# Performance work log

Measured on AMD Instinct MI355X. Metric: run time of the kernel, lower is better.

The kernel has to match this reference:

```python
import jax, jax.numpy as jnp
import numpy as np

NEG_SLOPE = 0.2  # PyG GATv2Conv default negative_slope


def gatv2_conv(x, src, dst, Wl, Wr, att, bias, concat):
    # x: [N, Fin]; src/dst: [E]; Wl/Wr: [Fin, H*C]; att: [H, C]
    N = x.shape[0]
    H, C = att.shape
    xl = (x @ Wl).reshape(N, H, C)
    xr = (x @ Wr).reshape(N, H, C)
    m = jax.nn.leaky_relu(xl[src] + xr[dst], NEG_SLOPE)          # [E,H,C]
    logits = jnp.einsum('ehc,hc->eh', m, att)                    # [E,H]
    lmax = jax.ops.segment_max(logits, dst, num_segments=N)      # stable softmax per dst segment
    ex = jnp.exp(logits - lmax[dst])
    denom = jax.ops.segment_sum(ex, dst, num_segments=N)
    alpha = ex / (denom[dst] + 1e-16)
    out = jax.ops.segment_sum(xl[src] * alpha[:, :, None], dst, num_segments=N)  # [N,H,C]
    out = out.reshape(N, H * C) if concat else out.mean(axis=1)
    return out + bias


def setup_inputs() -> dict:
    key = jax.random.key(0)
    ks = jax.random.split(key, 9)
    bsz, T, n_nodes = 8, 100, 2048
    Cin, hid, H, Cout = 128, 64, 4, 128
    inp = jax.random.normal(ks[0], (bsz, T, n_nodes), jnp.float32)
    ei = jax.random.randint(ks[1], (2, 32768), 0, n_nodes, jnp.int32)
    # remove self loops (PyG remove_self_loops before adding them back)
    ei = ei.at[1].set(jnp.where(ei[0] == ei[1], (ei[1] + 1) % n_nodes, ei[1]))

    def lin(k, fi, fo):
        return jax.random.normal(k, (fi, fo), jnp.float32) / np.sqrt(fi).astype(np.float32)

    return {
        'input': inp, 'edge_index': ei,
        'W_temb': lin(ks[2], T, Cin), 'b_temb': jnp.zeros((Cin,), jnp.float32),
        'Wl1': lin(ks[3], Cin, H * hid), 'Wr1': lin(ks[4], Cin, H * hid),
        'att1': jax.random.normal(ks[5], (H, hid), jnp.float32) / np.sqrt(hid).astype(np.float32),
        'b1': jnp.zeros((H * hid,), jnp.float32),
        'Wl2': lin(ks[6], H * hid, Cout), 'Wr2': lin(ks[7], H * hid, Cout),
        'att2': jax.random.normal(ks[8], (1, Cout), jnp.float32) / np.sqrt(Cout).astype(np.float32),
        'b2': jnp.zeros((Cout,), jnp.float32),
    }


def reference(input, edge_index, W_temb, b_temb, Wl1, Wr1, att1, b1, Wl2, Wr2, att2, b2):
    bsz, T, n_nodes = input.shape
    N = bsz * n_nodes
    # temporal embedding: [B,T,n] -> [B,n,T] @ [T,Cin] -> flatten to [N,Cin]
    x = (jnp.swapaxes(input, 1, 2) @ W_temb + b_temb).reshape(N, -1)
    # faithful to source: edge_index.repeat(1, bsz) tiles edges with NO batch offset;
    # GATv2Conv then adds self loops over all N nodes
    loops = jnp.arange(N, dtype=edge_index.dtype)
    src = jnp.concatenate([jnp.tile(edge_index[0], bsz), loops])
    dst = jnp.concatenate([jnp.tile(edge_index[1], bsz), loops])
    x = gatv2_conv(x, src, dst, Wl1, Wr1, att1, b1, True)
    x = jax.nn.elu(x)
    x = gatv2_conv(x, src, dst, Wl2, Wr2, att2, b2, False)
    return x.reshape(bsz, n_nodes, -1).mean(axis=1)  # [bsz, out_channels]
```

## Files before the change

### kernel.cpp

```cpp
#include <hip/hip_runtime.h>
#include <hip/hip_bf16.h>
#include <math.h>

#define NEG_SLOPE 0.2f

constexpr int BSZ = 8, T = 100, NN = 2048, N = BSZ * NN;
constexpr int CIN = 128, F1 = 256, F2 = 128;
constexpr int E = 32768;
constexpr int MAXDEG = 64;

typedef _Float16 f16x8 __attribute__((ext_vector_type(8)));
typedef float f32x4 __attribute__((ext_vector_type(4)));

__device__ inline float lrelu(float m) { return m > 0.f ? m : NEG_SLOPE * m; }
__device__ inline float eluf(float v) { return v > 0.f ? v : expm1f(v); }

__global__ __launch_bounds__(256) void k_prep(const float* __restrict__ Wt,
        const float* __restrict__ Wl1, const float* __restrict__ Wr1,
        const float* __restrict__ Wl2, const float* __restrict__ Wr2,
        const float* __restrict__ b2,
        _Float16* __restrict__ Tt, _Float16* __restrict__ T1l,
        _Float16* __restrict__ T1r, _Float16* __restrict__ T2l,
        _Float16* __restrict__ T2r, int* __restrict__ cnt, float* __restrict__ out) {
    __shared__ _Float16 tile[32][33];
    const int job = blockIdx.x;
    const int t = threadIdx.x;
    if (job == 144) {
        for (int i = t; i < NN; i += 256) cnt[i] = 0;
        for (int i = t; i < BSZ * F2; i += 256) out[i] = b2[i & (F2 - 1)];
        return;
    }
    int which, base;
    if (job < 16)       { which = 0; base = 0; }
    else if (job < 48)  { which = 1; base = 16; }
    else if (job < 80)  { which = 2; base = 48; }
    else if (job < 112) { which = 3; base = 80; }
    else                { which = 4; base = 112; }
    const int Ks[5] = {100, 128, 128, 256, 256};
    const int Kd[5] = {128, 128, 128, 256, 256};
    const int Nc[5] = {128, 256, 256, 128, 128};
    const float* Wsrc[5] = {Wt, Wl1, Wr1, Wl2, Wr2};
    _Float16* Wdst[5] = {Tt, T1l, T1r, T2l, T2r};
    int rel = job - base;
    int ks = Ks[which], kd = Kd[which], nc = Nc[which];
    int tilesN = nc / 32;
    int tk = (rel / tilesN) * 32, tn = (rel % tilesN) * 32;
    const float* src = Wsrc[which];
    _Float16* dst = Wdst[which];
    int tx = t & 31, ty = t >> 5;
    for (int r = ty; r < 32; r += 8)
        tile[r][tx] = (tk + r < ks) ? (_Float16)src[(tk + r) * nc + tn + tx] : (_Float16)0.f;
    __syncthreads();
    for (int r = ty; r < 32; r += 8)
        dst[(tn + r) * kd + tk + tx] = tile[tx][r];
}

__global__ __launch_bounds__(512) void k_gm1(const float* __restrict__ in,
        const _Float16* __restrict__ Tt, const float* __restrict__ bt,
        const _Float16* __restrict__ T1l, const _Float16* __restrict__ T1r,
        const float* __restrict__ b1, const _Float16* __restrict__ T2l,
        const int* __restrict__ ei, int* __restrict__ cnt, int* __restrict__ srcs,
        float* __restrict__ xl1, float* __restrict__ xr1, float* __restrict__ out) {
    const int t = threadIdx.x;
    if (blockIdx.x >= 512) {
        int i = (blockIdx.x - 512) * 512 + t;
        int d = ei[E + i];
        int slot = atomicAdd(&cnt[d], 1);
        if (slot < MAXDEG) srcs[d * MAXDEG + slot] = ei[i];
        return;
    }
    __shared__ __align__(16) char smem[8704 + 16896];
    _Float16* xt  = (_Float16*)smem;
    _Float16* inA = (_Float16*)(smem + 8704);
    const int wave = t >> 6, lane = t & 63;
    const int quad = lane >> 4, l15 = lane & 15;
    const int mat = wave >> 2, cg4 = wave & 3;
    const int row0 = blockIdx.x * 32;
    {
        const int b = row0 >> 11, node0 = row0 & (NN - 1);
        const float* ip = in + (size_t)b * T * NN + node0;
        #pragma unroll
        for (int it = 0; it < 8; ++it) {
            int idx = t + it * 512;
            int tt = idx >> 5, n = idx & 31;
            inA[n * 136 + tt] = (tt < T) ? (_Float16)ip[tt * NN + n] : (_Float16)0.f;
        }
    }
    __syncthreads();
    {
        const int wcol = wave * 16 + l15;
        f32x4 a0 = {0,0,0,0}, a1 = {0,0,0,0};
        #pragma unroll
        for (int kt = 0; kt < 128; kt += 32) {
            f16x8 af0 = *(const f16x8*)&inA[l15 * 136 + kt + quad * 8];
            f16x8 af1 = *(const f16x8*)&inA[(16 + l15) * 136 + kt + quad * 8];
            f16x8 bf  = *(const f16x8*)&Tt[wcol * 128 + kt + quad * 8];
            a0 = __builtin_amdgcn_mfma_f32_16x16x32_f16(af0, bf, a0, 0, 0, 0);
            a1 = __builtin_amdgcn_mfma_f32_16x16x32_f16(af1, bf, a1, 0, 0, 0);
        }
        float bv = bt[wcol];
        #pragma unroll
        for (int r = 0; r < 4; ++r) {
            xt[(quad * 4 + r) * 136 + wcol]      = (_Float16)(a0[r] + bv);
            xt[(16 + quad * 4 + r) * 136 + wcol] = (_Float16)(a1[r] + bv);
        }
    }
    __syncthreads();
    const int nmats = (row0 < NN) ? 2 : 1;
    f32x4 acc[2][4];
    #pragma unroll
    for (int s = 0; s < 2; ++s)
        #pragma unroll
        for (int c = 0; c < 4; ++c) acc[s][c] = (f32x4){0,0,0,0};
    if (mat < nmats) {
        const _Float16* Tm = mat ? T1r : T1l;
        #pragma unroll
        for (int kt = 0; kt < CIN; kt += 32) {
            f16x8 af0 = *(const f16x8*)&xt[l15 * 136 + kt + quad * 8];
            f16x8 af1 = *(const f16x8*)&xt[(16 + l15) * 136 + kt + quad * 8];
            #pragma unroll
            for (int ct = 0; ct < 4; ++ct) {
                int col = cg4 * 64 + ct * 16 + l15;
                f16x8 bf = *(const f16x8*)&Tm[col * CIN + kt + quad * 8];
                acc[0][ct] = __builtin_amdgcn_mfma_f32_16x16x32_f16(af0, bf, acc[0][ct], 0, 0, 0);
                acc[1][ct] = __builtin_amdgcn_mfma_f32_16x16x32_f16(af1, bf, acc[1][ct], 0, 0, 0);
            }
        }
    }
    if (row0 < NN) {
        float* dst = mat ? xr1 : xl1;
        #pragma unroll
        for (int s = 0; s < 2; ++s)
            #pragma unroll
            for (int ct = 0; ct < 4; ++ct) {
                int col = cg4 * 64 + ct * 16 + l15;
                #pragma unroll
                for (int r = 0; r < 4; ++r)
                    dst[(row0 + s * 16 + quad * 4 + r) * F1 + col] = acc[s][ct][r];
            }
        return;
    }
    _Float16* hrow = (_Float16*)(smem + 8704);
    if (mat == 0) {
        #pragma unroll
        for (int ct = 0; ct < 4; ++ct) {
            int col = cg4 * 64 + ct * 16 + l15;
            float bv = b1[col];
            #pragma unroll
            for (int s = 0; s < 2; ++s)
                #pragma unroll
                for (int r = 0; r < 4; ++r)
                    hrow[(s * 16 + quad * 4 + r) * 264 + col] =
                        (_Float16)eluf(acc[s][ct][r] + bv);
        }
    }
    __syncthreads();
    f32x4 c0 = {0,0,0,0}, c1 = {0,0,0,0};
    const int colw = wave * 16 + l15;
    #pragma unroll
    for (int kt = 0; kt < F1; kt += 32) {
        f16x8 a0 = *(const f16x8*)&hrow[l15 * 264 + kt + quad * 8];
        f16x8 a1 = *(const f16x8*)&hrow[(16 + l15) * 264 + kt + quad * 8];
        f16x8 bf = *(const f16x8*)&T2l[colw * F1 + kt + quad * 8];
        c0 = __builtin_amdgcn_mfma_f32_16x16x32_f16(a0, bf, c0, 0, 0, 0);
        c1 = __builtin_amdgcn_mfma_f32_16x16x32_f16(a1, bf, c1, 0, 0, 0);
    }
    float s8 = c0[0] + c0[1] + c0[2] + c0[3] + c1[0] + c1[1] + c1[2] + c1[3];
    s8 += __shfl_xor(s8, 16, 64);
    s8 += __shfl_xor(s8, 32, 64);
    if (quad == 0)
        atomicAdd(&out[(row0 >> 11) * F2 + colw], s8 * (1.0f / NN));
}

__global__ __launch_bounds__(256) void k_gat1(const int* __restrict__ cnt,
        const int* __restrict__ srcs, const float* __restrict__ xl1,
        const float* __restrict__ xr1, const float* __restrict__ att1,
        const float* __restrict__ b1, _Float16* __restrict__ h1h) {
    __shared__ float lacc[4][F1];
    __shared__ float ldn[4][4];
    const int t = threadIdx.x;
    const int wv = t >> 6, c = t & 63;
    const int d = blockIdx.x;
    int deg = cnt[d]; deg = deg < MAXDEG ? deg : MAXDEG;
    float b[4], at[4], sh[4], acc[4] = {0,0,0,0}, dnl[4] = {0,0,0,0};
    #pragma unroll
    for (int k = 0; k < 4; ++k) {
        b[k]  = xr1[d * F1 + c + 64 * k];
        at[k] = att1[c + 64 * k];
        sh[k] = lrelu(xl1[d * F1 + c + 64 * k] + b[k]) * at[k];
    }
    #pragma unroll
    for (int o = 32; o; o >>= 1) {
        #pragma unroll
        for (int k = 0; k < 4; ++k) sh[k] += __shfl_xor(sh[k], o, 64);
    }
    for (int e = wv; e < deg; e += 8) {
        bool v2 = (e + 4) < deg;
        int s  = srcs[d * MAXDEG + e];
        int s2 = v2 ? srcs[d * MAXDEG + e + 4] : s;
        float a[4], p[4], a2[4], p2[4];
        #pragma unroll
        for (int k = 0; k < 4; ++k) {
            a[k]  = xl1[s  * F1 + c + 64 * k];
            a2[k] = xl1[s2 * F1 + c + 64 * k];
        }
        #pragma unroll
        for (int k = 0; k < 4; ++k) {
            p[k]  = lrelu(a[k]  + b[k]) * at[k];
            p2[k] = lrelu(a2[k] + b[k]) * at[k];
        }
        #pragma unroll
        for (int o = 32; o; o >>= 1) {
            #pragma unroll
            for (int k = 0; k < 4; ++k) {
                p[k]  += __shfl_xor(p[k],  o, 64);
                p2[k] += __shfl_xor(p2[k], o, 64);
            }
        }
        #pragma unroll
        for (int k = 0; k < 4; ++k) {
            float w  = 8.0f * __expf(p[k] - sh[k]);
            float w2 = v2 ? 8.0f * __expf(p2[k] - sh[k]) : 0.f;
            dnl[k] += w + w2;
            acc[k] = fmaf(w, a[k], fmaf(w2, a2[k], acc[k]));
        }
    }
    #pragma unroll
    for (int k = 0; k < 4; ++k) lacc[wv][c + 64 * k] = acc[k];
    if (c < 4) ldn[wv][c] = dnl[c];
    __syncthreads();
    int f = t, h = t >> 6;
    float tot = xl1[d * F1 + f] + lacc[0][f] + lacc[1][f] + lacc[2][f] + lacc[3][f];
    float dnf = 1.0f + ldn[0][h] + ldn[1][h] + ldn[2][h] + ldn[3][h];
    h1h[(size_t)d * F1 + f] = (_Float16)eluf(tot / (dnf + 1e-16f) + b1[f]);
}

__global__ __launch_bounds__(256) void k_gm2loc(const _Float16* __restrict__ h1h,
        const _Float16* __restrict__ T2l, const _Float16* __restrict__ T2r,
        float* __restrict__ xl2, float* __restrict__ xr2) {
    const int t = threadIdx.x;
    const int wave = t >> 6, lane = t & 63;
    const int quad = lane >> 4, l15 = lane & 15;
    const int mat = wave >> 1, cg = wave & 1;
    const int row0 = blockIdx.x * 16;
    const _Float16* Tm = mat ? T2r : T2l;
    f32x4 acc[4];
    #pragma unroll
    for (int c = 0; c < 4; ++c) acc[c] = (f32x4){0,0,0,0};
    #pragma unroll
    for (int kt = 0; kt < F1; kt += 32) {
        f16x8 af = *(const f16x8*)&h1h[(size_t)(row0 + l15) * F1 + kt + quad * 8];
        #pragma unroll
        for (int ct = 0; ct < 4; ++ct) {
            int col = cg * 64 + ct * 16 + l15;
            f16x8 bf = *(const f16x8*)&Tm[col * F1 + kt + quad * 8];
            acc[ct] = __builtin_amdgcn_mfma_f32_16x16x32_f16(af, bf, acc[ct], 0, 0, 0);
        }
    }
    float* dst = mat ? xr2 : xl2;
    #pragma unroll
    for (int ct = 0; ct < 4; ++ct) {
        int col = cg * 64 + ct * 16 + l15;
        #pragma unroll
        for (int r = 0; r < 4; ++r)
            dst[(row0 + quad * 4 + r) * F2 + col] = acc[ct][r];
    }
}

__global__ __launch_bounds__(256) void k_gat2(const int* __restrict__ cnt,
        const int* __restrict__ srcs, const float* __restrict__ xl2,
        const float* __restrict__ xr2, const float* __restrict__ att2,
        float* __restrict__ acc2) {
    const int d = blockIdx.x;
    const int t = threadIdx.x;
    const int wv = t >> 6, c = t & 63;
    int deg = cnt[d]; deg = deg < MAXDEG ? deg : MAXDEG;
    float b0 = xr2[d * F2 + c], b1v = xr2[d * F2 + c + 64];
    float at0 = att2[c], at1 = att2[c + 64];
    float sh = lrelu(xl2[d * F2 + c] + b0) * at0 + lrelu(xl2[d * F2 + c + 64] + b1v) * at1;
    #pragma unroll
    for (int o = 32; o; o >>= 1) sh += __shfl_xor(sh, o, 64);
    float acc0 = 0.f, acc1v = 0.f, dnl = 0.f;
    for (int e = wv; e < deg; e += 8) {
        bool v2 = (e + 4) < deg;
        int s  = srcs[d * MAXDEG + e];
        int s2 = v2 ? srcs[d * MAXDEG + e + 4] : s;
        float a0 = xl2[s  * F2 + c], a1 = xl2[s  * F2 + c + 64];
        float e0 = xl2[s2 * F2 + c], e1 = xl2[s2 * F2 + c + 64];
        float p = lrelu(a0 + b0) * at0 + lrelu(a1 + b1v) * at1;
        float q = lrelu(e0 + b0) * at0 + lrelu(e1 + b1v) * at1;
        #pragma unroll
        for (int o = 32; o; o >>= 1) {
            p += __shfl_xor(p, o, 64);
            q += __shfl_xor(q, o, 64);
        }
        float w  = 8.0f * __expf(p - sh);
        float w2 = v2 ? 8.0f * __expf(q - sh) : 0.f;
        dnl += w + w2;
        acc0  = fmaf(w, a0, fmaf(w2, e0, acc0));
        acc1v = fmaf(w, a1, fmaf(w2, e1, acc1v));
    }
    __shared__ float lacc[4][F2];
    __shared__ float ldn[4];
    lacc[wv][c] = acc0;
    lacc[wv][c + 64] = acc1v;
    if (c == 0) ldn[wv] = dnl;
    __syncthreads();
    if (t < F2) {
        int f = t;
        float dnf = 1.0f + ldn[0] + ldn[1] + ldn[2] + ldn[3] + 1e-16f;
        acc2[d * F2 + f] =
            (xl2[d * F2 + f] + lacc[0][f] + lacc[1][f] + lacc[2][f] + lacc[3][f]) / dnf;
    }
}

__global__ __launch_bounds__(128) void k_out0(const float* __restrict__ acc2,
        float* __restrict__ out) {
    int chunk = blockIdx.x;
    int c = threadIdx.x;
    float s = 0.f;
    int n0 = chunk * 64;
    #pragma unroll 8
    for (int i = 0; i < 64; ++i)
        s += acc2[(n0 + i) * F2 + c];
    atomicAdd(&out[c], s * (1.0f / NN));
}

extern "C" void kernel_launch(void* const* d_in, const int* in_sizes, int n_in,
                              void* d_out, int out_size, void* d_ws, size_t ws_size,
                              hipStream_t stream) {
    const float* in   = (const float*)d_in[0];
    const int*   ei   = (const int*)d_in[1];
    const float* Wt   = (const float*)d_in[2];
    const float* bt   = (const float*)d_in[3];
    const float* Wl1  = (const float*)d_in[4];
    const float* Wr1  = (const float*)d_in[5];
    const float* att1 = (const float*)d_in[6];
    const float* b1   = (const float*)d_in[7];
    const float* Wl2  = (const float*)d_in[8];
    const float* Wr2  = (const float*)d_in[9];
    const float* att2 = (const float*)d_in[10];
    const float* b2   = (const float*)d_in[11];
    float* out = (float*)d_out;

    float* ws = (float*)d_ws;
    _Float16* h1h = (_Float16*)ws;
    float* xl1  = (float*)(h1h + (size_t)NN * F1);
    float* xr1  = xl1 + NN * F1;
    float* xl2  = xr1 + NN * F1;
    float* xr2  = xl2 + NN * F2;
    float* acc2 = xr2 + NN * F2;
    _Float16* Tt  = (_Float16*)(acc2 + NN * F2);
    _Float16* T1l = Tt + 128 * 128;
    _Float16* T1r = T1l + 256 * 128;
    _Float16* T2l = T1r + 256 * 128;
    _Float16* T2r = T2l + 128 * 256;
    int* cnt  = (int*)(T2r + 128 * 256);
    int* srcs = cnt + NN;

    k_prep<<<145, 256, 0, stream>>>(Wt, Wl1, Wr1, Wl2, Wr2, b2,
                                    Tt, T1l, T1r, T2l, T2r, cnt, out);
    k_gm1<<<576, 512, 0, stream>>>(in, Tt, bt, T1l, T1r, b1, T2l, ei, cnt, srcs,
                                   xl1, xr1, out);
    k_gat1<<<2048, 256, 0, stream>>>(cnt, srcs, xl1, xr1, att1, b1, h1h);
    k_gm2loc<<<128, 256, 0, stream>>>(h1h, T2l, T2r, xl2, xr2);
    k_gat2<<<NN, 256, 0, stream>>>(cnt, srcs, xl2, xr2, att2, acc2);
    k_out0<<<32, 128, 0, stream>>>(acc2, out);
}
```

Measured before the change: 133.6 us.

## Fuse GAT layer-1 aggregation with layer-2 projection and fold final mean into gat2

The layer-1 attention aggregation now runs in the same kernel as the layer-2 linear projection. Each wave aggregates two destination nodes and writes the ELU output to shared memory as fp16, which the MFMA projection then reads, so the global h1 buffer round trip goes away. The layer-2 aggregation kernel also absorbs the final node-mean. It accumulates into 32 bucketed partial sums and uses a last-block-done atomic counter to write the output, which removes the separate reduction kernel. The trade-off is much less parallelism in the layer-1 gather: 128 blocks, with each wave walking all edges serially instead of four waves splitting them. It also adds atomics and fences.

```diff
diff --git a/kernel.cpp b/kernel.cpp
--- a/kernel.cpp
+++ b/kernel.cpp
@@ -11,6 +11,8 @@
 
 typedef _Float16 f16x8 __attribute__((ext_vector_type(8)));
 typedef float f32x4 __attribute__((ext_vector_type(4)));
+
+#define MFMA16 __builtin_amdgcn_mfma_f32_16x16x32_f16
 
 __device__ inline float lrelu(float m) { return m > 0.f ? m : NEG_SLOPE * m; }
 __device__ inline float eluf(float v) { return v > 0.f ? v : expm1f(v); }
@@ -21,12 +23,16 @@
         const float* __restrict__ b2,
         _Float16* __restrict__ Tt, _Float16* __restrict__ T1l,
         _Float16* __restrict__ T1r, _Float16* __restrict__ T2l,
-        _Float16* __restrict__ T2r, int* __restrict__ cnt, float* __restrict__ out) {
+        _Float16* __restrict__ T2r, int* __restrict__ cnt,
+        float* __restrict__ part32, int* __restrict__ done32,
+        float* __restrict__ out) {
     __shared__ _Float16 tile[32][33];
     const int job = blockIdx.x;
     const int t = threadIdx.x;
     if (job == 144) {
         for (int i = t; i < NN; i += 256) cnt[i] = 0;
+        for (int i = t; i < 32 * F2; i += 256) part32[i] = 0.f;
+        if (t < 33) done32[t] = 0;
         for (int i = t; i < BSZ * F2; i += 256) out[i] = b2[i & (F2 - 1)];
         return;
     }
@@ -95,8 +101,8 @@
             f16x8 af0 = *(const f16x8*)&inA[l15 * 136 + kt + quad * 8];
             f16x8 af1 = *(const f16x8*)&inA[(16 + l15) * 136 + kt + quad * 8];
             f16x8 bf  = *(const f16x8*)&Tt[wcol * 128 + kt + quad * 8];
-            a0 = __builtin_amdgcn_mfma_f32_16x16x32_f16(af0, bf, a0, 0, 0, 0);
-            a1 = __builtin_amdgcn_mfma_f32_16x16x32_f16(af1, bf, a1, 0, 0, 0);
+            a0 = MFMA16(af0, bf, a0, 0, 0, 0);
+            a1 = MFMA16(af1, bf, a1, 0, 0, 0);
         }
         float bv = bt[wcol];
         #pragma unroll
@@ -122,8 +128,8 @@
             for (int ct = 0; ct < 4; ++ct) {
                 int col = cg4 * 64 + ct * 16 + l15;
                 f16x8 bf = *(const f16x8*)&Tm[col * CIN + kt + quad * 8];
-                acc[0][ct] = __builtin_amdgcn_mfma_f32_16x16x32_f16(af0, bf, acc[0][ct], 0, 0, 0);
-                acc[1][ct] = __builtin_amdgcn_mfma_f32_16x16x32_f16(af1, bf, acc[1][ct], 0, 0, 0);
+                acc[0][ct] = MFMA16(af0, bf, acc[0][ct], 0, 0, 0);
+                acc[1][ct] = MFMA16(af1, bf, acc[1][ct], 0, 0, 0);
             }
         }
     }
@@ -162,8 +168,8 @@
         f16x8 a0 = *(const f16x8*)&hrow[l15 * 264 + kt + quad * 8];
         f16x8 a1 = *(const f16x8*)&hrow[(16 + l15) * 264 + kt + quad * 8];
         f16x8 bf = *(const f16x8*)&T2l[colw * F1 + kt + quad * 8];
-        c0 = __builtin_amdgcn_mfma_f32_16x16x32_f16(a0, bf, c0, 0, 0, 0);
-        c1 = __builtin_amdgcn_mfma_f32_16x16x32_f16(a1, bf, c1, 0, 0, 0);
+        c0 = MFMA16(a0, bf, c0, 0, 0, 0);
+        c1 = MFMA16(a1, bf, c1, 0, 0, 0);
     }
     float s8 = c0[0] + c0[1] + c0[2] + c0[3] + c1[0] + c1[1] + c1[2] + c1[3];
     s8 += __shfl_xor(s8, 16, 64);
@@ -172,105 +178,100 @@
         atomicAdd(&out[(row0 >> 11) * F2 + colw], s8 * (1.0f / NN));
 }
 
-__global__ __launch_bounds__(256) void k_gat1(const int* __restrict__ cnt,
+__global__ __launch_bounds__(512) void k_gat1g2(const int* __restrict__ cnt,
         const int* __restrict__ srcs, const float* __restrict__ xl1,
         const float* __restrict__ xr1, const float* __restrict__ att1,
-        const float* __restrict__ b1, _Float16* __restrict__ h1h) {
-    __shared__ float lacc[4][F1];
-    __shared__ float ldn[4][4];
-    const int t = threadIdx.x;
-    const int wv = t >> 6, c = t & 63;
-    const int d = blockIdx.x;
-    int deg = cnt[d]; deg = deg < MAXDEG ? deg : MAXDEG;
-    float b[4], at[4], sh[4], acc[4] = {0,0,0,0}, dnl[4] = {0,0,0,0};
-    #pragma unroll
-    for (int k = 0; k < 4; ++k) {
-        b[k]  = xr1[d * F1 + c + 64 * k];
-        at[k] = att1[c + 64 * k];
-        sh[k] = lrelu(xl1[d * F1 + c + 64 * k] + b[k]) * at[k];
-    }
-    #pragma unroll
-    for (int o = 32; o; o >>= 1) {
-        #pragma unroll
-        for (int k = 0; k < 4; ++k) sh[k] += __shfl_xor(sh[k], o, 64);
-    }
-    for (int e = wv; e < deg; e += 8) {
-        bool v2 = (e + 4) < deg;
-        int s  = srcs[d * MAXDEG + e];
-        int s2 = v2 ? srcs[d * MAXDEG + e + 4] : s;
-        float a[4], p[4], a2[4], p2[4];
-        #pragma unroll
-        for (int k = 0; k < 4; ++k) {
-            a[k]  = xl1[s  * F1 + c + 64 * k];
-            a2[k] = xl1[s2 * F1 + c + 64 * k];
-        }
-        #pragma unroll
-        for (int k = 0; k < 4; ++k) {
-            p[k]  = lrelu(a[k]  + b[k]) * at[k];
-            p2[k] = lrelu(a2[k] + b[k]) * at[k];
-        }
-        #pragma unroll
-        for (int o = 32; o; o >>= 1) {
-            #pragma unroll
-            for (int k = 0; k < 4; ++k) {
-                p[k]  += __shfl_xor(p[k],  o, 64);
-                p2[k] += __shfl_xor(p2[k], o, 64);
-            }
-        }
-        #pragma unroll
-        for (int k = 0; k < 4; ++k) {
-            float w  = 8.0f * __expf(p[k] - sh[k]);
-            float w2 = v2 ? 8.0f * __expf(p2[k] - sh[k]) : 0.f;
-            dnl[k] += w + w2;
-            acc[k] = fmaf(w, a[k], fmaf(w2, a2[k], acc[k]));
-        }
-    }
-    #pragma unroll
-    for (int k = 0; k < 4; ++k) lacc[wv][c + 64 * k] = acc[k];
-    if (c < 4) ldn[wv][c] = dnl[c];
-    __syncthreads();
-    int f = t, h = t >> 6;
-    float tot = xl1[d * F1 + f] + lacc[0][f] + lacc[1][f] + lacc[2][f] + lacc[3][f];
-    float dnf = 1.0f + ldn[0][h] + ldn[1][h] + ldn[2][h] + ldn[3][h];
-    h1h[(size_t)d * F1 + f] = (_Float16)eluf(tot / (dnf + 1e-16f) + b1[f]);
-}
-
-__global__ __launch_bounds__(256) void k_gm2loc(const _Float16* __restrict__ h1h,
-        const _Float16* __restrict__ T2l, const _Float16* __restrict__ T2r,
+        const float* __restrict__ b1, const _Float16* __restrict__ T2l,
+        const _Float16* __restrict__ T2r,
         float* __restrict__ xl2, float* __restrict__ xr2) {
+    __shared__ _Float16 hrow[16][264];
     const int t = threadIdx.x;
     const int wave = t >> 6, lane = t & 63;
     const int quad = lane >> 4, l15 = lane & 15;
-    const int mat = wave >> 1, cg = wave & 1;
-    const int row0 = blockIdx.x * 16;
+    const int node0 = blockIdx.x * 16;
+    const int c = lane;
+    #pragma unroll
+    for (int rep = 0; rep < 2; ++rep) {
+        const int d = node0 + wave * 2 + rep;
+        int deg = cnt[d]; deg = deg < MAXDEG ? deg : MAXDEG;
+        float bb[4], at[4], aself[4], shl[4], acc[4] = {0,0,0,0}, dnl[4] = {0,0,0,0};
+        #pragma unroll
+        for (int k = 0; k < 4; ++k) {
+            bb[k]    = xr1[d * F1 + c + 64 * k];
+            at[k]    = att1[c + 64 * k];
+            aself[k] = xl1[d * F1 + c + 64 * k];
+            shl[k]   = lrelu(aself[k] + bb[k]) * at[k];
+        }
+        #pragma unroll
+        for (int o = 32; o; o >>= 1) {
+            #pragma unroll
+            for (int k = 0; k < 4; ++k) shl[k] += __shfl_xor(shl[k], o, 64);
+        }
+        for (int e = 0; e < deg; e += 2) {
+            bool v2 = (e + 1) < deg;
+            int s  = srcs[d * MAXDEG + e];
+            int s2 = v2 ? srcs[d * MAXDEG + e + 1] : s;
+            float a[4], p[4], a2[4], p2[4];
+            #pragma unroll
+            for (int k = 0; k < 4; ++k) {
+                a[k]  = xl1[s  * F1 + c + 64 * k];
+                a2[k] = xl1[s2 * F1 + c + 64 * k];
+            }
+            #pragma unroll
+            for (int k = 0; k < 4; ++k) {
+                p[k]  = lrelu(a[k]  + bb[k]) * at[k];
+                p2[k] = lrelu(a2[k] + bb[k]) * at[k];
+            }
+            #pragma unroll
+            for (int o = 32; o; o >>= 1) {
+                #pragma unroll
+                for (int k = 0; k < 4; ++k) {
+                    p[k]  += __shfl_xor(p[k],  o, 64);
+                    p2[k] += __shfl_xor(p2[k], o, 64);
+                }
+            }
+            #pragma unroll
+            for (int k = 0; k < 4; ++k) {
+                float w  = 8.0f * __expf(p[k] - shl[k]);
+                float w2 = v2 ? 8.0f * __expf(p2[k] - shl[k]) : 0.f;
+                dnl[k] += w + w2;
+                acc[k] = fmaf(w, a[k], fmaf(w2, a2[k], acc[k]));
+            }
+        }
+        #pragma unroll
+        for (int k = 0; k < 4; ++k) {
+            float dnf = 1.0f + dnl[k] + 1e-16f;
+            float val = eluf((aself[k] + acc[k]) / dnf + b1[c + 64 * k]);
+            hrow[wave * 2 + rep][c + 64 * k] = (_Float16)val;
+        }
+    }
+    __syncthreads();
+    const int mat = wave >> 2, cg = wave & 3;
     const _Float16* Tm = mat ? T2r : T2l;
-    f32x4 acc[4];
-    #pragma unroll
-    for (int c = 0; c < 4; ++c) acc[c] = (f32x4){0,0,0,0};
+    f32x4 a0 = {0,0,0,0}, a1 = {0,0,0,0};
     #pragma unroll
     for (int kt = 0; kt < F1; kt += 32) {
-        f16x8 af = *(const f16x8*)&h1h[(size_t)(row0 + l15) * F1 + kt + quad * 8];
-        #pragma unroll
-        for (int ct = 0; ct < 4; ++ct) {
-            int col = cg * 64 + ct * 16 + l15;
-            f16x8 bf = *(const f16x8*)&Tm[col * F1 + kt + quad * 8];
-            acc[ct] = __builtin_amdgcn_mfma_f32_16x16x32_f16(af, bf, acc[ct], 0, 0, 0);
-        }
+        f16x8 af  = *(const f16x8*)&hrow[l15][kt + quad * 8];
+        int col0 = cg * 32 + l15;
+        f16x8 bf0 = *(const f16x8*)&Tm[col0 * F1 + kt + quad * 8];
+        f16x8 bf1 = *(const f16x8*)&Tm[(col0 + 16) * F1 + kt + quad * 8];
+        a0 = MFMA16(af, bf0, a0, 0, 0, 0);
+        a1 = MFMA16(af, bf1, a1, 0, 0, 0);
     }
     float* dst = mat ? xr2 : xl2;
-    #pragma unroll
-    for (int ct = 0; ct < 4; ++ct) {
-        int col = cg * 64 + ct * 16 + l15;
-        #pragma unroll
-        for (int r = 0; r < 4; ++r)
-            dst[(row0 + quad * 4 + r) * F2 + col] = acc[ct][r];
-    }
-}
-
-__global__ __launch_bounds__(256) void k_gat2(const int* __restrict__ cnt,
+    int col0 = cg * 32 + l15;
+    #pragma unroll
+    for (int r = 0; r < 4; ++r) {
+        dst[(node0 + quad * 4 + r) * F2 + col0]      = a0[r];
+        dst[(node0 + quad * 4 + r) * F2 + col0 + 16] = a1[r];
+    }
+}
+
+__global__ __launch_bounds__(256) void k_gat2fin(const int* __restrict__ cnt,
         const int* __restrict__ srcs, const float* __restrict__ xl2,
         const float* __restrict__ xr2, const float* __restrict__ att2,
-        float* __restrict__ acc2) {
+        const float* __restrict__ b2, float* __restrict__ part32,
+        int* __restrict__ done32, float* __restrict__ out) {
     const int d = blockIdx.x;
     const int t = threadIdx.x;
     const int wv = t >> 6, c = t & 63;
@@ -302,28 +303,41 @@
     }
     __shared__ float lacc[4][F2];
     __shared__ float ldn[4];
+    __shared__ int role;
     lacc[wv][c] = acc0;
     lacc[wv][c + 64] = acc1v;
     if (c == 0) ldn[wv] = dnl;
     __syncthreads();
+    const int bkt = d & 31;
     if (t < F2) {
-        int f = t;
         float dnf = 1.0f + ldn[0] + ldn[1] + ldn[2] + ldn[3] + 1e-16f;
-        acc2[d * F2 + f] =
-            (xl2[d * F2 + f] + lacc[0][f] + lacc[1][f] + lacc[2][f] + lacc[3][f]) / dnf;
-    }
-}
-
-__global__ __launch_bounds__(128) void k_out0(const float* __restrict__ acc2,
-        float* __restrict__ out) {
-    int chunk = blockIdx.x;
-    int c = threadIdx.x;
-    float s = 0.f;
-    int n0 = chunk * 64;
-    #pragma unroll 8
-    for (int i = 0; i < 64; ++i)
-        s += acc2[(n0 + i) * F2 + c];
-    atomicAdd(&out[c], s * (1.0f / NN));
+        float v = (xl2[d * F2 + t] + lacc[0][t] + lacc[1][t] + lacc[2][t] + lacc[3][t]) / dnf;
+        atomicAdd(&part32[bkt * F2 + t], v * (1.0f / NN));
+    }
+    __threadfence();
+    __syncthreads();
+    if (t == 0) {
+        int old = __hip_atomic_fetch_add(&done32[bkt], 1, __ATOMIC_ACQ_REL,
+                                         __HIP_MEMORY_SCOPE_AGENT);
+        role = (old == 63) ? 1 : 0;
+    }
+    __syncthreads();
+    if (!role) return;
+    if (t == 0) {
+        int old2 = __hip_atomic_fetch_add(&done32[32], 1, __ATOMIC_ACQ_REL,
+                                          __HIP_MEMORY_SCOPE_AGENT);
+        role = (old2 == 31) ? 2 : 0;
+    }
+    __syncthreads();
+    if (role != 2) return;
+    if (t < F2) {
+        float s = 0.f;
+        #pragma unroll 8
+        for (int k = 0; k < 32; ++k)
+            s += __hip_atomic_load(&part32[k * F2 + t], __ATOMIC_RELAXED,
+                                   __HIP_MEMORY_SCOPE_AGENT);
+        out[t] = b2[t] + s;
+    }
 }
 
 extern "C" void kernel_launch(void* const* d_in, const int* in_sizes, int n_in,
@@ -344,26 +358,26 @@
     float* out = (float*)d_out;
 
     float* ws = (float*)d_ws;
-    _Float16* h1h = (_Float16*)ws;
-    float* xl1  = (float*)(h1h + (size_t)NN * F1);
+    float* xl1  = ws;
     float* xr1  = xl1 + NN * F1;
     float* xl2  = xr1 + NN * F1;
     float* xr2  = xl2 + NN * F2;
-    float* acc2 = xr2 + NN * F2;
-    _Float16* Tt  = (_Float16*)(acc2 + NN * F2);
+    float* part32 = xr2 + NN * F2;
+    _Float16* Tt  = (_Float16*)(part32 + 32 * F2);
     _Float16* T1l = Tt + 128 * 128;
     _Float16* T1r = T1l + 256 * 128;
     _Float16* T2l = T1r + 256 * 128;
     _Float16* T2r = T2l + 128 * 256;
-    int* cnt  = (int*)(T2r + 128 * 256);
-    int* srcs = cnt + NN;
+    int* cnt    = (int*)(T2r + 128 * 256);
+    int* done32 = cnt + NN;
+    int* srcs   = done32 + 64;
 
     k_prep<<<145, 256, 0, stream>>>(Wt, Wl1, Wr1, Wl2, Wr2, b2,
-                                    Tt, T1l, T1r, T2l, T2r, cnt, out);
+                                    Tt, T1l, T1r, T2l, T2r, cnt, part32, done32, out);
     k_gm1<<<576, 512, 0, stream>>>(in, Tt, bt, T1l, T1r, b1, T2l, ei, cnt, srcs,
                                    xl1, xr1, out);
-    k_gat1<<<2048, 256, 0, stream>>>(cnt, srcs, xl1, xr1, att1, b1, h1h);
-    k_gm2loc<<<128, 256, 0, stream>>>(h1h, T2l, T2r, xl2, xr2);
-    k_gat2<<<NN, 256, 0, stream>>>(cnt, srcs, xl2, xr2, att2, acc2);
-    k_out0<<<32, 128, 0, stream>>>(acc2, out);
-}
+    k_gat1g2<<<128, 512, 0, stream>>>(cnt, srcs, xl1, xr1, att1, b1, T2l, T2r,
+                                      xl2, xr2);
+    k_gat2fin<<<NN, 256, 0, stream>>>(cnt, srcs, xl2, xr2, att2, b2,
+                                      part32, done32, out);
+}
```

New measurement: 293.5 us. 120% more time.
